# Kernel optimization log

Measured on AMD Instinct MI355X. Metric: run time of the kernel, lower is better.

Reference implementation:

```python
import jax, jax.numpy as jnp
import numpy as np
import math

ROPE_BASE = 10000.0
ALIBI_SLOPE = 2.0 ** (-8.0)  # _get_alibi_slopes(1) == [2**(-8*1/1)]


def _rope_cos_sin(T, d):
    inv_freq = 1.0 / (ROPE_BASE ** (jnp.arange(0, d, 2, dtype=jnp.float32) / d))
    t = jnp.arange(T, dtype=jnp.float32)
    freqs = jnp.einsum('i,j->ij', t, inv_freq)          # [T, d/2]
    emb = jnp.concatenate([freqs, freqs], axis=-1)      # [T, d]
    return jnp.cos(emb), jnp.sin(emb)


def _rotate_half(x):
    x1, x2 = jnp.split(x, 2, axis=-1)
    return jnp.concatenate([-x2, x1], axis=-1)


def setup_inputs() -> dict:
    key = jax.random.key(0)
    kq, kk, kv = jax.random.split(key, 3)
    B, T, H = 8, 2048, 256
    return {
        'q': jax.random.normal(kq, (B, T, H), dtype=jnp.float32),
        'k': jax.random.normal(kk, (B, T, H), dtype=jnp.float32),
        'v': jax.random.normal(kv, (B, T, H), dtype=jnp.float32),
    }


def reference(q, k, v):
    B, T, H = q.shape  # num_heads == 1, so head_dim == H
    cos, sin = _rope_cos_sin(T, H)                      # [T, H]
    qe = q * cos + _rotate_half(q) * sin                # [B, T, H]
    ke = k * cos + _rotate_half(k) * sin                # [B, T, H]

    scale = 1.0 / math.sqrt(H)
    scores = jnp.einsum('btd,bsd->bts', qe, ke) * scale  # [B, T, T]

    pos = jnp.arange(T)
    rel = (pos[None, :] - pos[:, None]).astype(jnp.float32)  # [T, T]
    alibi = (ALIBI_SLOPE * rel)[None, None, :, :]            # [1, 1, T, T]

    # torch broadcast: [B,T,T] + [1,1,T,T] -> [1,B,T,T]
    scores = scores + alibi
    attn = jax.nn.softmax(scores, axis=-1)              # [1, B, T, T]
    out = jnp.matmul(attn, v)                           # [1, B, T, H]
    return out
```

## Files before the change

kernel.cpp:

```cpp
#include <hip/hip_runtime.h>

#define B_ 8
#define T_ 2048
#define H_ 256
#define PSTR 40
#define SCALE2 0.0901684403f
#define SLOPE2 0.00563552752f
#define ELEMS ((size_t)B_ * T_ * H_)

typedef __attribute__((ext_vector_type(8))) short bf16x8;
typedef __attribute__((ext_vector_type(4))) float f32x4;

#define MFMA16(a, b, c) __builtin_amdgcn_mfma_f32_16x16x32_bf16((a), (b), (c), 0, 0, 0)

__device__ __forceinline__ ushort f2bf(float f) {
  unsigned u = __float_as_uint(f);
  u += 0x7FFFu + ((u >> 16) & 1u);
  return (ushort)(u >> 16);
}

__device__ __forceinline__ void gl_lds16(const ushort* g, ushort* l) {
  __builtin_amdgcn_global_load_lds(
      (const __attribute__((address_space(1))) unsigned int*)g,
      (__attribute__((address_space(3))) unsigned int*)l, 16, 0, 0);
}

__global__ void prep_kernel(const float* __restrict__ k, const float* __restrict__ v,
                            ushort* __restrict__ kt, ushort* __restrict__ vt) {
  __shared__ ushort tile[64][72];
  const int bid = blockIdx.x;
  const int tid = threadIdx.x;
  if (bid < 1024) {
    int idx = bid * 256 + tid;
    int d8 = idx & 15;
    int bt = idx >> 4;
    int t = bt & (T_ - 1);
    int b = bt >> 11;
    size_t base = (size_t)bt * H_ + d8 * 8;
    float4 a0 = *(const float4*)(k + base);
    float4 a1 = *(const float4*)(k + base + 4);
    float4 c0 = *(const float4*)(k + base + 128);
    float4 c1 = *(const float4*)(k + base + 132);
    float av[8] = {a0.x, a0.y, a0.z, a0.w, a1.x, a1.y, a1.z, a1.w};
    float cv[8] = {c0.x, c0.y, c0.z, c0.w, c1.x, c1.y, c1.z, c1.w};
    bf16x8 lo, hi;
#pragma unroll
    for (int e = 0; e < 8; ++e) {
      int j = d8 * 8 + e;
      float rv = (float)t * exp2f((float)j * -0.103810252959f) * 0.15915494309f;
      float fr = rv - floorf(rv);
      float sn = __builtin_amdgcn_sinf(fr), cs = __builtin_amdgcn_cosf(fr);
      lo[e] = (short)f2bf(av[e] * cs - cv[e] * sn);
      hi[e] = (short)f2bf(cv[e] * cs + av[e] * sn);
    }
    size_t kdst = (((size_t)(b * 64 + (t >> 5)) * 32 + d8) * 32 + (t & 31)) * 8;
    *(bf16x8*)(kt + kdst) = lo;
    *(bf16x8*)(kt + kdst + 4096) = hi;
  } else {
    int bid2 = bid - 1024;
    int b = bid2 >> 7, rem = bid2 & 127;
    int h0 = (rem >> 5) * 64, t0 = (rem & 31) * 64;
    int c4 = tid & 15, r0 = tid >> 4;
#pragma unroll
    for (int p = 0; p < 4; ++p) {
      int row = r0 + p * 16;
      const float4 f = *(const float4*)(v + ((size_t)(b * T_ + t0 + row)) * H_ + h0 + c4 * 4);
      ushort4 u;
      u.x = f2bf(f.x); u.y = f2bf(f.y); u.z = f2bf(f.z); u.w = f2bf(f.w);
      *(ushort4*)&tile[row][(c4 * 4) ^ (8 * ((row >> 3) & 7))] = u;
    }
    __syncthreads();
#pragma unroll
    for (int p = 0; p < 2; ++p) {
      int c = tid + p * 256;
      int h = c >> 3, tc = (c & 7) * 8;
      int xo = 8 * (c & 7);
      ushort4 u0, u1;
      u0.x = tile[tc + 0][h ^ xo]; u0.y = tile[tc + 1][h ^ xo];
      u0.z = tile[tc + 2][h ^ xo]; u0.w = tile[tc + 3][h ^ xo];
      u1.x = tile[tc + 4][h ^ xo]; u1.y = tile[tc + 5][h ^ xo];
      u1.z = tile[tc + 6][h ^ xo]; u1.w = tile[tc + 7][h ^ xo];
      int tg = t0 + tc;
      size_t dst = (((size_t)(b * 64 + (tg >> 5)) * 4 + ((tg >> 3) & 3)) * 256 + (h0 + h)) * 8;
      *(ushort4*)(vt + dst) = u0;
      *(ushort4*)(vt + dst + 4) = u1;
    }
  }
}

__global__ __launch_bounds__(512, 4)
void attn_kernel(const float* __restrict__ q, const ushort* __restrict__ kt,
                 const ushort* __restrict__ vt, float* __restrict__ out,
                 float* __restrict__ opart, float* __restrict__ lpart) {
  __shared__ ushort Ksh[2][8192];
  __shared__ ushort Vsh[2][8192];
  __shared__ ushort Psh[8][16 * PSTR];

  const int tid = threadIdx.x;
  const int w = tid >> 6, lane = tid & 63, quad = lane >> 4, l16 = lane & 15;
  const int b = blockIdx.x;
  const int q0 = blockIdx.y * 128;
  const int sp = blockIdx.z;
  const int S = gridDim.z;
  const int niter = (T_ / 32) / S;
  const int kvb = sp * (T_ / S);

  bf16x8 aq[8];
  {
    const float* qb = q + ((size_t)(b * T_) + q0 + w * 16) * H_;
    const int t = q0 + w * 16 + l16;
    float qv[8][8];
#pragma unroll
    for (int ks = 0; ks < 8; ++ks) {
      float4 x0 = *(const float4*)(qb + (size_t)l16 * H_ + ks * 32 + quad * 8);
      float4 x1 = *(const float4*)(qb + (size_t)l16 * H_ + ks * 32 + quad * 8 + 4);
      qv[ks][0] = x0.x; qv[ks][1] = x0.y; qv[ks][2] = x0.z; qv[ks][3] = x0.w;
      qv[ks][4] = x1.x; qv[ks][5] = x1.y; qv[ks][6] = x1.z; qv[ks][7] = x1.w;
    }
#pragma unroll
    for (int ks = 0; ks < 4; ++ks)
#pragma unroll
      for (int e = 0; e < 8; ++e) {
        int d = ks * 32 + quad * 8 + e;
        float rv = (float)t * exp2f((float)d * -0.103810252959f) * 0.15915494309f;
        float fr = rv - floorf(rv);
        float sn = __builtin_amdgcn_sinf(fr), cs = __builtin_amdgcn_cosf(fr);
        aq[ks][e]     = (short)f2bf(qv[ks][e] * cs - qv[ks + 4][e] * sn);
        aq[ks + 4][e] = (short)f2bf(qv[ks + 4][e] * cs + qv[ks][e] * sn);
      }
  }

  const f32x4 fzero = {0.f, 0.f, 0.f, 0.f};
  f32x4 O[16], lac = fzero;
#pragma unroll
  for (int ht = 0; ht < 16; ++ht) O[ht] = fzero;
  bf16x8 vones;
#pragma unroll
  for (int i = 0; i < 8; ++i) vones[i] = (short)0x3F80;

  const ushort* ktb = kt + (size_t)(b * 64 + sp * niter) * 8192;
  const ushort* vtb = vt + (size_t)(b * 64 + sp * niter) * 8192;
  const int stoff = tid * 8;

#pragma unroll
  for (int tt = 0; tt < 2; ++tt) {
    const ushort* kg = ktb + (size_t)tt * 8192;
    const ushort* vg = vtb + (size_t)tt * 8192;
    gl_lds16(kg + stoff, &Ksh[tt][stoff]);
    gl_lds16(kg + stoff + 4096, &Ksh[tt][stoff + 4096]);
    gl_lds16(vg + stoff, &Vsh[tt][stoff]);
    gl_lds16(vg + stoff + 4096, &Vsh[tt][stoff + 4096]);
  }

  const float arb = SLOPE2 * (float)(q0 + w * 16 + quad * 4);

  for (int it = 0; it < niter; ++it) {
    const int p = it & 1;
    __builtin_amdgcn_sched_barrier(0);
    if (it == niter - 1) __builtin_amdgcn_s_waitcnt(0x0070);
    else                 __builtin_amdgcn_s_waitcnt(0x0F74);
    __builtin_amdgcn_s_barrier();
    __builtin_amdgcn_sched_barrier(0);

    f32x4 s[2] = {fzero, fzero};
#pragma unroll
    for (int ks = 0; ks < 8; ++ks)
#pragma unroll
      for (int nt = 0; nt < 2; ++nt) {
        bf16x8 kf = *(const bf16x8*)&Ksh[p][((ks * 4 + quad) * 32 + nt * 16 + l16) * 8];
        s[nt] = MFMA16(aq[ks], kf, s[nt]);
      }

#pragma unroll
    for (int nt = 0; nt < 2; ++nt) {
      float ac = SLOPE2 * (float)(kvb + it * 32 + nt * 16 + l16);
#pragma unroll
      for (int r = 0; r < 4; ++r) {
        float a0 = ac - arb - SLOPE2 * (float)r;
        float pv = __builtin_amdgcn_exp2f(fmaf(s[nt][r], SCALE2, a0));
        Psh[w][(quad * 4 + r) * PSTR + nt * 16 + l16] = f2bf(pv);
      }
    }

    bf16x8 pf = *(const bf16x8*)&Psh[w][l16 * PSTR + quad * 8];
    lac = MFMA16(pf, vones, lac);
#pragma unroll
    for (int ht = 0; ht < 16; ++ht) {
      bf16x8 vf = *(const bf16x8*)&Vsh[p][(quad * 256 + ht * 16 + l16) * 8];
      O[ht] = MFMA16(pf, vf, O[ht]);
    }

    __builtin_amdgcn_sched_barrier(0);
    __builtin_amdgcn_s_waitcnt(0xC07F);
    __builtin_amdgcn_s_barrier();
    __builtin_amdgcn_sched_barrier(0);

    if (it < niter - 2) {
      const ushort* kg = ktb + (size_t)(it + 2) * 8192;
      const ushort* vg = vtb + (size_t)(it + 2) * 8192;
      gl_lds16(kg + stoff, &Ksh[p][stoff]);
      gl_lds16(kg + stoff + 4096, &Ksh[p][stoff + 4096]);
      gl_lds16(vg + stoff, &Vsh[p][stoff]);
      gl_lds16(vg + stoff + 4096, &Vsh[p][stoff + 4096]);
    }
  }

  float* od = (sp == 0) ? out : (opart + (size_t)(sp - 1) * ELEMS);
  float* ob = od + ((size_t)(b * T_) + q0 + w * 16) * H_;
#pragma unroll
  for (int r = 0; r < 4; ++r) {
    int row = quad * 4 + r;
#pragma unroll
    for (int ht = 0; ht < 16; ++ht)
      ob[(size_t)row * H_ + ht * 16 + l16] = O[ht][r];
  }
  if (l16 == 0) {
#pragma unroll
    for (int r = 0; r < 4; ++r)
      lpart[(size_t)(sp * B_ + b) * T_ + q0 + w * 16 + quad * 4 + r] = lac[r];
  }
}

__global__ void combine_kernel(float* __restrict__ out, const float* __restrict__ opart,
                               const float* __restrict__ lpart, int S) {
  int idx = blockIdx.x * 256 + threadIdx.x;
  int row = idx >> 6;
  float l = lpart[row];
  for (int s = 1; s < S; ++s) l += lpart[(size_t)s * B_ * T_ + row];
  float inv = 1.0f / l;
  float4 a = ((const float4*)out)[idx];
  for (int s = 1; s < S; ++s) {
    float4 c = ((const float4*)opart)[(size_t)(s - 1) * (ELEMS / 4) + idx];
    a.x += c.x; a.y += c.y; a.z += c.z; a.w += c.w;
  }
  a.x *= inv; a.y *= inv; a.z *= inv; a.w *= inv;
  ((float4*)out)[idx] = a;
}

extern "C" void kernel_launch(void* const* d_in, const int* in_sizes, int n_in,
                              void* d_out, int out_size, void* d_ws, size_t ws_size,
                              hipStream_t stream) {
  const float* q = (const float*)d_in[0];
  const float* k = (const float*)d_in[1];
  const float* v = (const float*)d_in[2];
  float* out = (float*)d_out;

  ushort* kt = (ushort*)d_ws;
  ushort* vt = kt + ELEMS;
  float* opart = (float*)(vt + ELEMS);
  const size_t need4 = ELEMS * 4 + 3 * ELEMS * 4 + (size_t)4 * B_ * T_ * 4;
  const int S = (ws_size >= need4) ? 4 : 2;
  float* lpart = opart + (size_t)(S - 1) * ELEMS;

  prep_kernel<<<dim3(2048), 256, 0, stream>>>(k, v, kt, vt);
  attn_kernel<<<dim3(B_, T_ / 128, S), 512, 0, stream>>>(q, kt, vt, out, opart, lpart);
  combine_kernel<<<dim3((B_ * T_ * H_ / 4) / 256), 256, 0, stream>>>(out, opart, lpart, S);
}
```

Measured before the change: 153.4 us.

## Split KV range across wave groups inside block and merge in LDS, dropping combine kernel

The attention kernel now processes 64 query rows per block, with two groups of four waves each covering half of the KV sequence. The two partial outputs and row sums are merged through shared memory, and the result is written directly. This removes the partial-output workspace traffic and the separate combine kernel launch. In exchange it uses about 138 KB of LDS per block, so only one block fits per CU, and the grid is 2048 blocks with less latency hiding across blocks.

```diff
diff --git a/kernel.cpp b/kernel.cpp
--- a/kernel.cpp
+++ b/kernel.cpp
@@ -88,27 +88,33 @@
   }
 }
 
-__global__ __launch_bounds__(512, 4)
+__global__ __launch_bounds__(512, 1)
 void attn_kernel(const float* __restrict__ q, const ushort* __restrict__ kt,
-                 const ushort* __restrict__ vt, float* __restrict__ out,
-                 float* __restrict__ opart, float* __restrict__ lpart) {
-  __shared__ ushort Ksh[2][8192];
-  __shared__ ushort Vsh[2][8192];
-  __shared__ ushort Psh[8][16 * PSTR];
+                 const ushort* __restrict__ vt, float* __restrict__ out) {
+  __shared__ __align__(16) char smem[141568];
+  ushort* Kbase = (ushort*)smem;
+  ushort* Vbase = (ushort*)(smem + 65536);
+  ushort* Pbase = (ushort*)(smem + 131072);
+  float*  Lsh   = (float*)(smem + 141312);
+  float*  Ofl   = (float*)smem;
 
   const int tid = threadIdx.x;
   const int w = tid >> 6, lane = tid & 63, quad = lane >> 4, l16 = lane & 15;
+  const int g = w >> 2;
+  const int wl = w & 3;
+  const int gt = tid & 255;
   const int b = blockIdx.x;
-  const int q0 = blockIdx.y * 128;
-  const int sp = blockIdx.z;
-  const int S = gridDim.z;
-  const int niter = (T_ / 32) / S;
-  const int kvb = sp * (T_ / S);
+  const int q0 = blockIdx.y * 64;
+  const int kvb0 = g * (T_ / 2);
+
+  ushort* Ksh = Kbase + g * 16384;
+  ushort* Vsh = Vbase + g * 16384;
+  ushort* Psh = Pbase + w * (16 * PSTR);
 
   bf16x8 aq[8];
   {
-    const float* qb = q + ((size_t)(b * T_) + q0 + w * 16) * H_;
-    const int t = q0 + w * 16 + l16;
+    const float* qb = q + ((size_t)(b * T_) + q0 + wl * 16) * H_;
+    const int t = q0 + wl * 16 + l16;
     float qv[8][8];
 #pragma unroll
     for (int ks = 0; ks < 8; ++ks) {
@@ -138,27 +144,28 @@
 #pragma unroll
   for (int i = 0; i < 8; ++i) vones[i] = (short)0x3F80;
 
-  const ushort* ktb = kt + (size_t)(b * 64 + sp * niter) * 8192;
-  const ushort* vtb = vt + (size_t)(b * 64 + sp * niter) * 8192;
-  const int stoff = tid * 8;
+  const ushort* ktb = kt + (size_t)(b * 64 + g * 32) * 8192;
+  const ushort* vtb = vt + (size_t)(b * 64 + g * 32) * 8192;
+  const int stoff = gt * 8;
 
 #pragma unroll
   for (int tt = 0; tt < 2; ++tt) {
     const ushort* kg = ktb + (size_t)tt * 8192;
     const ushort* vg = vtb + (size_t)tt * 8192;
-    gl_lds16(kg + stoff, &Ksh[tt][stoff]);
-    gl_lds16(kg + stoff + 4096, &Ksh[tt][stoff + 4096]);
-    gl_lds16(vg + stoff, &Vsh[tt][stoff]);
-    gl_lds16(vg + stoff + 4096, &Vsh[tt][stoff + 4096]);
-  }
-
-  const float arb = SLOPE2 * (float)(q0 + w * 16 + quad * 4);
-
-  for (int it = 0; it < niter; ++it) {
+#pragma unroll
+    for (int i = 0; i < 4; ++i) {
+      gl_lds16(kg + stoff + i * 2048, Ksh + tt * 8192 + stoff + i * 2048);
+      gl_lds16(vg + stoff + i * 2048, Vsh + tt * 8192 + stoff + i * 2048);
+    }
+  }
+
+  const float arb = SLOPE2 * (float)(q0 + wl * 16 + quad * 4);
+
+  for (int it = 0; it < 32; ++it) {
     const int p = it & 1;
     __builtin_amdgcn_sched_barrier(0);
-    if (it == niter - 1) __builtin_amdgcn_s_waitcnt(0x0070);
-    else                 __builtin_amdgcn_s_waitcnt(0x0F74);
+    if (it == 31) __builtin_amdgcn_s_waitcnt(0x0070);
+    else          __builtin_amdgcn_s_waitcnt(0x0F78);
     __builtin_amdgcn_s_barrier();
     __builtin_amdgcn_sched_barrier(0);
 
@@ -167,26 +174,26 @@
     for (int ks = 0; ks < 8; ++ks)
 #pragma unroll
       for (int nt = 0; nt < 2; ++nt) {
-        bf16x8 kf = *(const bf16x8*)&Ksh[p][((ks * 4 + quad) * 32 + nt * 16 + l16) * 8];
+        bf16x8 kf = *(const bf16x8*)&Ksh[p * 8192 + ((ks * 4 + quad) * 32 + nt * 16 + l16) * 8];
         s[nt] = MFMA16(aq[ks], kf, s[nt]);
       }
 
 #pragma unroll
     for (int nt = 0; nt < 2; ++nt) {
-      float ac = SLOPE2 * (float)(kvb + it * 32 + nt * 16 + l16);
+      float ac = SLOPE2 * (float)(kvb0 + it * 32 + nt * 16 + l16);
 #pragma unroll
       for (int r = 0; r < 4; ++r) {
         float a0 = ac - arb - SLOPE2 * (float)r;
         float pv = __builtin_amdgcn_exp2f(fmaf(s[nt][r], SCALE2, a0));
-        Psh[w][(quad * 4 + r) * PSTR + nt * 16 + l16] = f2bf(pv);
-      }
-    }
-
-    bf16x8 pf = *(const bf16x8*)&Psh[w][l16 * PSTR + quad * 8];
+        Psh[(quad * 4 + r) * PSTR + nt * 16 + l16] = f2bf(pv);
+      }
+    }
+
+    bf16x8 pf = *(const bf16x8*)&Psh[l16 * PSTR + quad * 8];
     lac = MFMA16(pf, vones, lac);
 #pragma unroll
     for (int ht = 0; ht < 16; ++ht) {
-      bf16x8 vf = *(const bf16x8*)&Vsh[p][(quad * 256 + ht * 16 + l16) * 8];
+      bf16x8 vf = *(const bf16x8*)&Vsh[p * 8192 + (quad * 256 + ht * 16 + l16) * 8];
       O[ht] = MFMA16(pf, vf, O[ht]);
     }
 
@@ -195,46 +202,40 @@
     __builtin_amdgcn_s_barrier();
     __builtin_amdgcn_sched_barrier(0);
 
-    if (it < niter - 2) {
+    if (it < 30) {
       const ushort* kg = ktb + (size_t)(it + 2) * 8192;
       const ushort* vg = vtb + (size_t)(it + 2) * 8192;
-      gl_lds16(kg + stoff, &Ksh[p][stoff]);
-      gl_lds16(kg + stoff + 4096, &Ksh[p][stoff + 4096]);
-      gl_lds16(vg + stoff, &Vsh[p][stoff]);
-      gl_lds16(vg + stoff + 4096, &Vsh[p][stoff + 4096]);
-    }
-  }
-
-  float* od = (sp == 0) ? out : (opart + (size_t)(sp - 1) * ELEMS);
-  float* ob = od + ((size_t)(b * T_) + q0 + w * 16) * H_;
-#pragma unroll
-  for (int r = 0; r < 4; ++r) {
-    int row = quad * 4 + r;
-#pragma unroll
-    for (int ht = 0; ht < 16; ++ht)
-      ob[(size_t)row * H_ + ht * 16 + l16] = O[ht][r];
-  }
-  if (l16 == 0) {
-#pragma unroll
-    for (int r = 0; r < 4; ++r)
-      lpart[(size_t)(sp * B_ + b) * T_ + q0 + w * 16 + quad * 4 + r] = lac[r];
-  }
-}
-
-__global__ void combine_kernel(float* __restrict__ out, const float* __restrict__ opart,
-                               const float* __restrict__ lpart, int S) {
-  int idx = blockIdx.x * 256 + threadIdx.x;
-  int row = idx >> 6;
-  float l = lpart[row];
-  for (int s = 1; s < S; ++s) l += lpart[(size_t)s * B_ * T_ + row];
-  float inv = 1.0f / l;
-  float4 a = ((const float4*)out)[idx];
-  for (int s = 1; s < S; ++s) {
-    float4 c = ((const float4*)opart)[(size_t)(s - 1) * (ELEMS / 4) + idx];
-    a.x += c.x; a.y += c.y; a.z += c.z; a.w += c.w;
-  }
-  a.x *= inv; a.y *= inv; a.z *= inv; a.w *= inv;
-  ((float4*)out)[idx] = a;
+#pragma unroll
+      for (int i = 0; i < 4; ++i) {
+        gl_lds16(kg + stoff + i * 2048, Ksh + p * 8192 + stoff + i * 2048);
+        gl_lds16(vg + stoff + i * 2048, Vsh + p * 8192 + stoff + i * 2048);
+      }
+    }
+  }
+
+  if (g == 1) {
+#pragma unroll
+    for (int r = 0; r < 4; ++r) {
+      int row = wl * 16 + quad * 4 + r;
+#pragma unroll
+      for (int ht = 0; ht < 16; ++ht)
+        Ofl[row * 260 + ht * 16 + l16] = O[ht][r];
+      if (l16 == 0) Lsh[row] = lac[r];
+    }
+  }
+  __syncthreads();
+  if (g == 0) {
+    float* ob = out + ((size_t)(b * T_) + q0 + wl * 16) * H_;
+#pragma unroll
+    for (int r = 0; r < 4; ++r) {
+      int row = wl * 16 + quad * 4 + r;
+      float inv = 1.0f / (lac[r] + Lsh[row]);
+#pragma unroll
+      for (int ht = 0; ht < 16; ++ht)
+        ob[(size_t)(quad * 4 + r) * H_ + ht * 16 + l16] =
+            (O[ht][r] + Ofl[row * 260 + ht * 16 + l16]) * inv;
+    }
+  }
 }
 
 extern "C" void kernel_launch(void* const* d_in, const int* in_sizes, int n_in,
@@ -247,12 +248,7 @@
 
   ushort* kt = (ushort*)d_ws;
   ushort* vt = kt + ELEMS;
-  float* opart = (float*)(vt + ELEMS);
-  const size_t need4 = ELEMS * 4 + 3 * ELEMS * 4 + (size_t)4 * B_ * T_ * 4;
-  const int S = (ws_size >= need4) ? 4 : 2;
-  float* lpart = opart + (size_t)(S - 1) * ELEMS;
 
   prep_kernel<<<dim3(2048), 256, 0, stream>>>(k, v, kt, vt);
-  attn_kernel<<<dim3(B_, T_ / 128, S), 512, 0, stream>>>(q, kt, vt, out, opart, lpart);
-  combine_kernel<<<dim3((B_ * T_ * H_ / 4) / 256), 256, 0, stream>>>(out, opart, lpart, S);
-}
+  attn_kernel<<<dim3(B_, T_ / 64), 512, 0, stream>>>(q, kt, vt, out);
+}
```

New measurement: 144.6 us. 5.7% less time.

## Double KV tile to 64 keys and fix split-K at two partitions

Applied to the files above, without the earlier changes.

Each attention iteration now processes 64 keys instead of 32, doubling the K/V LDS buffers (about 64KB each for double buffering) and the P scratch stride. The split-K factor is hardwired to 2, which halves the partial-output traffic and simplifies the combine kernel. The intent is fewer barriers and waits per key and less combine memory traffic. The cost is higher LDS usage, which cuts occupancy (launch bounds drop to 2 blocks per SM), and fewer blocks in the grid.

```diff
diff --git a/kernel.cpp b/kernel.cpp
--- a/kernel.cpp
+++ b/kernel.cpp
@@ -3,7 +3,7 @@
 #define B_ 8
 #define T_ 2048
 #define H_ 256
-#define PSTR 40
+#define PSTR 72
 #define SCALE2 0.0901684403f
 #define SLOPE2 0.00563552752f
 #define ELEMS ((size_t)B_ * T_ * H_)
@@ -88,12 +88,12 @@
   }
 }
 
-__global__ __launch_bounds__(512, 4)
+__global__ __launch_bounds__(512, 2)
 void attn_kernel(const float* __restrict__ q, const ushort* __restrict__ kt,
                  const ushort* __restrict__ vt, float* __restrict__ out,
-                 float* __restrict__ opart, float* __restrict__ lpart) {
-  __shared__ ushort Ksh[2][8192];
-  __shared__ ushort Vsh[2][8192];
+                 float* __restrict__ o1, float* __restrict__ lpart) {
+  __shared__ ushort Ksh[2][16384];
+  __shared__ ushort Vsh[2][16384];
   __shared__ ushort Psh[8][16 * PSTR];
 
   const int tid = threadIdx.x;
@@ -101,9 +101,8 @@
   const int b = blockIdx.x;
   const int q0 = blockIdx.y * 128;
   const int sp = blockIdx.z;
-  const int S = gridDim.z;
-  const int niter = (T_ / 32) / S;
-  const int kvb = sp * (T_ / S);
+  const int kvb = sp * (T_ / 2);
+  const int niter = 16;
 
   bf16x8 aq[8];
   {
@@ -138,18 +137,19 @@
 #pragma unroll
   for (int i = 0; i < 8; ++i) vones[i] = (short)0x3F80;
 
-  const ushort* ktb = kt + (size_t)(b * 64 + sp * niter) * 8192;
-  const ushort* vtb = vt + (size_t)(b * 64 + sp * niter) * 8192;
+  const ushort* ktb = kt + (size_t)(b * 64 + sp * 32) * 8192;
+  const ushort* vtb = vt + (size_t)(b * 64 + sp * 32) * 8192;
   const int stoff = tid * 8;
 
 #pragma unroll
   for (int tt = 0; tt < 2; ++tt) {
-    const ushort* kg = ktb + (size_t)tt * 8192;
-    const ushort* vg = vtb + (size_t)tt * 8192;
-    gl_lds16(kg + stoff, &Ksh[tt][stoff]);
-    gl_lds16(kg + stoff + 4096, &Ksh[tt][stoff + 4096]);
-    gl_lds16(vg + stoff, &Vsh[tt][stoff]);
-    gl_lds16(vg + stoff + 4096, &Vsh[tt][stoff + 4096]);
+    const ushort* kg = ktb + (size_t)tt * 16384;
+    const ushort* vg = vtb + (size_t)tt * 16384;
+#pragma unroll
+    for (int i = 0; i < 4; ++i) {
+      gl_lds16(kg + stoff + i * 4096, &Ksh[tt][stoff + i * 4096]);
+      gl_lds16(vg + stoff + i * 4096, &Vsh[tt][stoff + i * 4096]);
+    }
   }
 
   const float arb = SLOPE2 * (float)(q0 + w * 16 + quad * 4);
@@ -158,22 +158,23 @@
     const int p = it & 1;
     __builtin_amdgcn_sched_barrier(0);
     if (it == niter - 1) __builtin_amdgcn_s_waitcnt(0x0070);
-    else                 __builtin_amdgcn_s_waitcnt(0x0F74);
+    else                 __builtin_amdgcn_s_waitcnt(0x0F78);
     __builtin_amdgcn_s_barrier();
     __builtin_amdgcn_sched_barrier(0);
 
-    f32x4 s[2] = {fzero, fzero};
+    f32x4 s[4] = {fzero, fzero, fzero, fzero};
 #pragma unroll
     for (int ks = 0; ks < 8; ++ks)
 #pragma unroll
-      for (int nt = 0; nt < 2; ++nt) {
-        bf16x8 kf = *(const bf16x8*)&Ksh[p][((ks * 4 + quad) * 32 + nt * 16 + l16) * 8];
+      for (int nt = 0; nt < 4; ++nt) {
+        bf16x8 kf = *(const bf16x8*)&Ksh[p][(nt >> 1) * 8192 +
+            ((ks * 4 + quad) * 32 + (nt & 1) * 16 + l16) * 8];
         s[nt] = MFMA16(aq[ks], kf, s[nt]);
       }
 
 #pragma unroll
-    for (int nt = 0; nt < 2; ++nt) {
-      float ac = SLOPE2 * (float)(kvb + it * 32 + nt * 16 + l16);
+    for (int nt = 0; nt < 4; ++nt) {
+      float ac = SLOPE2 * (float)(kvb + it * 64 + nt * 16 + l16);
 #pragma unroll
       for (int r = 0; r < 4; ++r) {
         float a0 = ac - arb - SLOPE2 * (float)r;
@@ -182,12 +183,16 @@
       }
     }
 
-    bf16x8 pf = *(const bf16x8*)&Psh[w][l16 * PSTR + quad * 8];
-    lac = MFMA16(pf, vones, lac);
+    bf16x8 pf0 = *(const bf16x8*)&Psh[w][l16 * PSTR + quad * 8];
+    bf16x8 pf1 = *(const bf16x8*)&Psh[w][l16 * PSTR + 32 + quad * 8];
+    lac = MFMA16(pf0, vones, lac);
+    lac = MFMA16(pf1, vones, lac);
 #pragma unroll
     for (int ht = 0; ht < 16; ++ht) {
-      bf16x8 vf = *(const bf16x8*)&Vsh[p][(quad * 256 + ht * 16 + l16) * 8];
-      O[ht] = MFMA16(pf, vf, O[ht]);
+      bf16x8 vf0 = *(const bf16x8*)&Vsh[p][(quad * 256 + ht * 16 + l16) * 8];
+      bf16x8 vf1 = *(const bf16x8*)&Vsh[p][8192 + (quad * 256 + ht * 16 + l16) * 8];
+      O[ht] = MFMA16(pf0, vf0, O[ht]);
+      O[ht] = MFMA16(pf1, vf1, O[ht]);
     }
 
     __builtin_amdgcn_sched_barrier(0);
@@ -196,16 +201,17 @@
     __builtin_amdgcn_sched_barrier(0);
 
     if (it < niter - 2) {
-      const ushort* kg = ktb + (size_t)(it + 2) * 8192;
-      const ushort* vg = vtb + (size_t)(it + 2) * 8192;
-      gl_lds16(kg + stoff, &Ksh[p][stoff]);
-      gl_lds16(kg + stoff + 4096, &Ksh[p][stoff + 4096]);
-      gl_lds16(vg + stoff, &Vsh[p][stoff]);
-      gl_lds16(vg + stoff + 4096, &Vsh[p][stoff + 4096]);
-    }
-  }
-
-  float* od = (sp == 0) ? out : (opart + (size_t)(sp - 1) * ELEMS);
+      const ushort* kg = ktb + (size_t)(it + 2) * 16384;
+      const ushort* vg = vtb + (size_t)(it + 2) * 16384;
+#pragma unroll
+      for (int i = 0; i < 4; ++i) {
+        gl_lds16(kg + stoff + i * 4096, &Ksh[p][stoff + i * 4096]);
+        gl_lds16(vg + stoff + i * 4096, &Vsh[p][stoff + i * 4096]);
+      }
+    }
+  }
+
+  float* od = (sp == 0) ? out : o1;
   float* ob = od + ((size_t)(b * T_) + q0 + w * 16) * H_;
 #pragma unroll
   for (int r = 0; r < 4; ++r) {
@@ -221,19 +227,15 @@
   }
 }
 
-__global__ void combine_kernel(float* __restrict__ out, const float* __restrict__ opart,
-                               const float* __restrict__ lpart, int S) {
+__global__ void combine_kernel(float* __restrict__ out, const float* __restrict__ o1,
+                               const float* __restrict__ lpart) {
   int idx = blockIdx.x * 256 + threadIdx.x;
   int row = idx >> 6;
-  float l = lpart[row];
-  for (int s = 1; s < S; ++s) l += lpart[(size_t)s * B_ * T_ + row];
-  float inv = 1.0f / l;
+  float inv = 1.0f / (lpart[row] + lpart[B_ * T_ + row]);
   float4 a = ((const float4*)out)[idx];
-  for (int s = 1; s < S; ++s) {
-    float4 c = ((const float4*)opart)[(size_t)(s - 1) * (ELEMS / 4) + idx];
-    a.x += c.x; a.y += c.y; a.z += c.z; a.w += c.w;
-  }
-  a.x *= inv; a.y *= inv; a.z *= inv; a.w *= inv;
+  float4 c = ((const float4*)o1)[idx];
+  a.x = (a.x + c.x) * inv; a.y = (a.y + c.y) * inv;
+  a.z = (a.z + c.z) * inv; a.w = (a.w + c.w) * inv;
   ((float4*)out)[idx] = a;
 }
 
@@ -247,12 +249,10 @@
 
   ushort* kt = (ushort*)d_ws;
   ushort* vt = kt + ELEMS;
-  float* opart = (float*)(vt + ELEMS);
-  const size_t need4 = ELEMS * 4 + 3 * ELEMS * 4 + (size_t)4 * B_ * T_ * 4;
-  const int S = (ws_size >= need4) ? 4 : 2;
-  float* lpart = opart + (size_t)(S - 1) * ELEMS;
+  float* o1 = (float*)(vt + ELEMS);
+  float* lpart = o1 + ELEMS;
 
   prep_kernel<<<dim3(2048), 256, 0, stream>>>(k, v, kt, vt);
-  attn_kernel<<<dim3(B_, T_ / 128, S), 512, 0, stream>>>(q, kt, vt, out, opart, lpart);
-  combine_kernel<<<dim3((B_ * T_ * H_ / 4) / 256), 256, 0, stream>>>(out, opart, lpart, S);
-}
+  attn_kernel<<<dim3(B_, T_ / 128, 2), 512, 0, stream>>>(q, kt, vt, out, o1, lpart);
+  combine_kernel<<<dim3((B_ * T_ * H_ / 4) / 256), 256, 0, stream>>>(out, o1, lpart);
+}
```

Result: faster. 145.5 us (-5.2%).

## Switch attention to 32x32x16 MFMA with 32-row query tiles per wave

Applied to the files above, without the earlier changes.

Each wave now handles 32 query rows with the 32x32x16 bf16 MFMA instead of 16 rows with 16x16x32. Each block covers 256 queries, halving the grid along T and halving how often each K/V tile is streamed into LDS per query. This raises MFMA work per LDS load. In exchange the accumulator registers roughly double, so launch bounds drop to 2 blocks per SM, which lowers occupancy and the latency hiding it gives.

```diff
diff --git a/kernel.cpp b/kernel.cpp
--- a/kernel.cpp
+++ b/kernel.cpp
@@ -10,8 +10,9 @@
 
 typedef __attribute__((ext_vector_type(8))) short bf16x8;
 typedef __attribute__((ext_vector_type(4))) float f32x4;
-
-#define MFMA16(a, b, c) __builtin_amdgcn_mfma_f32_16x16x32_bf16((a), (b), (c), 0, 0, 0)
+typedef __attribute__((ext_vector_type(16))) float f32x16;
+
+#define MFMA32(a, b, c) __builtin_amdgcn_mfma_f32_32x32x16_bf16((a), (b), (c), 0, 0, 0)
 
 __device__ __forceinline__ ushort f2bf(float f) {
   unsigned u = __float_as_uint(f);
@@ -88,58 +89,62 @@
   }
 }
 
-__global__ __launch_bounds__(512, 4)
+__global__ __launch_bounds__(512, 2)
 void attn_kernel(const float* __restrict__ q, const ushort* __restrict__ kt,
                  const ushort* __restrict__ vt, float* __restrict__ out,
                  float* __restrict__ opart, float* __restrict__ lpart) {
   __shared__ ushort Ksh[2][8192];
   __shared__ ushort Vsh[2][8192];
-  __shared__ ushort Psh[8][16 * PSTR];
+  __shared__ ushort Psh[8][32 * PSTR];
 
   const int tid = threadIdx.x;
-  const int w = tid >> 6, lane = tid & 63, quad = lane >> 4, l16 = lane & 15;
+  const int w = tid >> 6, lane = tid & 63;
+  const int l31 = lane & 31, lh = lane >> 5;
   const int b = blockIdx.x;
-  const int q0 = blockIdx.y * 128;
+  const int q0 = blockIdx.y * 256;
   const int sp = blockIdx.z;
   const int S = gridDim.z;
   const int niter = (T_ / 32) / S;
   const int kvb = sp * (T_ / S);
 
-  bf16x8 aq[8];
+  bf16x8 aq[16];
   {
-    const float* qb = q + ((size_t)(b * T_) + q0 + w * 16) * H_;
-    const int t = q0 + w * 16 + l16;
-    float qv[8][8];
+    const float* qb = q + ((size_t)(b * T_) + q0 + w * 32 + l31) * H_;
+    const float tq = (float)(q0 + w * 32 + l31);
 #pragma unroll
     for (int ks = 0; ks < 8; ++ks) {
-      float4 x0 = *(const float4*)(qb + (size_t)l16 * H_ + ks * 32 + quad * 8);
-      float4 x1 = *(const float4*)(qb + (size_t)l16 * H_ + ks * 32 + quad * 8 + 4);
-      qv[ks][0] = x0.x; qv[ks][1] = x0.y; qv[ks][2] = x0.z; qv[ks][3] = x0.w;
-      qv[ks][4] = x1.x; qv[ks][5] = x1.y; qv[ks][6] = x1.z; qv[ks][7] = x1.w;
-    }
-#pragma unroll
-    for (int ks = 0; ks < 4; ++ks)
+      const float* pl = qb + ks * 16 + lh * 8;
+      float4 x0 = *(const float4*)(pl);
+      float4 x1 = *(const float4*)(pl + 4);
+      float4 y0 = *(const float4*)(pl + 128);
+      float4 y1 = *(const float4*)(pl + 132);
+      float lo[8] = {x0.x, x0.y, x0.z, x0.w, x1.x, x1.y, x1.z, x1.w};
+      float hi[8] = {y0.x, y0.y, y0.z, y0.w, y1.x, y1.y, y1.z, y1.w};
 #pragma unroll
       for (int e = 0; e < 8; ++e) {
-        int d = ks * 32 + quad * 8 + e;
-        float rv = (float)t * exp2f((float)d * -0.103810252959f) * 0.15915494309f;
+        int d = ks * 16 + lh * 8 + e;
+        float rv = tq * exp2f((float)d * -0.103810252959f) * 0.15915494309f;
         float fr = rv - floorf(rv);
         float sn = __builtin_amdgcn_sinf(fr), cs = __builtin_amdgcn_cosf(fr);
-        aq[ks][e]     = (short)f2bf(qv[ks][e] * cs - qv[ks + 4][e] * sn);
-        aq[ks + 4][e] = (short)f2bf(qv[ks + 4][e] * cs + qv[ks][e] * sn);
+        aq[ks][e]     = (short)f2bf(lo[e] * cs - hi[e] * sn);
+        aq[ks + 8][e] = (short)f2bf(hi[e] * cs + lo[e] * sn);
       }
-  }
-
-  const f32x4 fzero = {0.f, 0.f, 0.f, 0.f};
-  f32x4 O[16], lac = fzero;
-#pragma unroll
-  for (int ht = 0; ht < 16; ++ht) O[ht] = fzero;
+    }
+  }
+
+  f32x16 fz16;
+#pragma unroll
+  for (int i = 0; i < 16; ++i) fz16[i] = 0.f;
+  f32x16 O[8], lac;
+#pragma unroll
+  for (int hb = 0; hb < 8; ++hb) O[hb] = fz16;
+  lac = fz16;
   bf16x8 vones;
 #pragma unroll
   for (int i = 0; i < 8; ++i) vones[i] = (short)0x3F80;
 
-  const ushort* ktb = kt + (size_t)(b * 64 + sp * niter) * 8192;
-  const ushort* vtb = vt + (size_t)(b * 64 + sp * niter) * 8192;
+  const ushort* ktb = kt + (size_t)(b * 64 + sp * (64 / S)) * 8192;
+  const ushort* vtb = vt + (size_t)(b * 64 + sp * (64 / S)) * 8192;
   const int stoff = tid * 8;
 
 #pragma unroll
@@ -152,7 +157,7 @@
     gl_lds16(vg + stoff + 4096, &Vsh[tt][stoff + 4096]);
   }
 
-  const float arb = SLOPE2 * (float)(q0 + w * 16 + quad * 4);
+  const float arb2 = SLOPE2 * (float)(q0 + w * 32);
 
   for (int it = 0; it < niter; ++it) {
     const int p = it & 1;
@@ -162,32 +167,33 @@
     __builtin_amdgcn_s_barrier();
     __builtin_amdgcn_sched_barrier(0);
 
-    f32x4 s[2] = {fzero, fzero};
-#pragma unroll
-    for (int ks = 0; ks < 8; ++ks)
-#pragma unroll
-      for (int nt = 0; nt < 2; ++nt) {
-        bf16x8 kf = *(const bf16x8*)&Ksh[p][((ks * 4 + quad) * 32 + nt * 16 + l16) * 8];
-        s[nt] = MFMA16(aq[ks], kf, s[nt]);
+    f32x16 s = fz16;
+#pragma unroll
+    for (int ks = 0; ks < 16; ++ks) {
+      bf16x8 kf = *(const bf16x8*)&Ksh[p][(((ks * 2 + lh) * 32) + l31) * 8];
+      s = MFMA32(aq[ks], kf, s);
+    }
+
+    {
+      float ac = SLOPE2 * (float)(kvb + it * 32 + l31) - arb2;
+#pragma unroll
+      for (int r = 0; r < 16; ++r) {
+        int row = (r & 3) + 8 * (r >> 2) + 4 * lh;
+        float pv = __builtin_amdgcn_exp2f(fmaf(s[r], SCALE2, ac - SLOPE2 * (float)row));
+        Psh[w][row * PSTR + l31] = f2bf(pv);
       }
-
-#pragma unroll
-    for (int nt = 0; nt < 2; ++nt) {
-      float ac = SLOPE2 * (float)(kvb + it * 32 + nt * 16 + l16);
-#pragma unroll
-      for (int r = 0; r < 4; ++r) {
-        float a0 = ac - arb - SLOPE2 * (float)r;
-        float pv = __builtin_amdgcn_exp2f(fmaf(s[nt][r], SCALE2, a0));
-        Psh[w][(quad * 4 + r) * PSTR + nt * 16 + l16] = f2bf(pv);
-      }
-    }
-
-    bf16x8 pf = *(const bf16x8*)&Psh[w][l16 * PSTR + quad * 8];
-    lac = MFMA16(pf, vones, lac);
-#pragma unroll
-    for (int ht = 0; ht < 16; ++ht) {
-      bf16x8 vf = *(const bf16x8*)&Vsh[p][(quad * 256 + ht * 16 + l16) * 8];
-      O[ht] = MFMA16(pf, vf, O[ht]);
+    }
+
+    bf16x8 pf0 = *(const bf16x8*)&Psh[w][l31 * PSTR + lh * 8];
+    bf16x8 pf1 = *(const bf16x8*)&Psh[w][l31 * PSTR + 16 + lh * 8];
+    lac = MFMA32(pf0, vones, lac);
+    lac = MFMA32(pf1, vones, lac);
+#pragma unroll
+    for (int hb = 0; hb < 8; ++hb) {
+      bf16x8 vf0 = *(const bf16x8*)&Vsh[p][((lh * 256) + hb * 32 + l31) * 8];
+      bf16x8 vf1 = *(const bf16x8*)&Vsh[p][(((2 + lh) * 256) + hb * 32 + l31) * 8];
+      O[hb] = MFMA32(pf0, vf0, O[hb]);
+      O[hb] = MFMA32(pf1, vf1, O[hb]);
     }
 
     __builtin_amdgcn_sched_barrier(0);
@@ -206,18 +212,20 @@
   }
 
   float* od = (sp == 0) ? out : (opart + (size_t)(sp - 1) * ELEMS);
-  float* ob = od + ((size_t)(b * T_) + q0 + w * 16) * H_;
-#pragma unroll
-  for (int r = 0; r < 4; ++r) {
-    int row = quad * 4 + r;
-#pragma unroll
-    for (int ht = 0; ht < 16; ++ht)
-      ob[(size_t)row * H_ + ht * 16 + l16] = O[ht][r];
-  }
-  if (l16 == 0) {
-#pragma unroll
-    for (int r = 0; r < 4; ++r)
-      lpart[(size_t)(sp * B_ + b) * T_ + q0 + w * 16 + quad * 4 + r] = lac[r];
+  float* ob = od + ((size_t)(b * T_) + q0 + w * 32) * H_;
+#pragma unroll
+  for (int r = 0; r < 16; ++r) {
+    int row = (r & 3) + 8 * (r >> 2) + 4 * lh;
+#pragma unroll
+    for (int hb = 0; hb < 8; ++hb)
+      ob[(size_t)row * H_ + hb * 32 + l31] = O[hb][r];
+  }
+  if (l31 == 0) {
+#pragma unroll
+    for (int r = 0; r < 16; ++r) {
+      int row = (r & 3) + 8 * (r >> 2) + 4 * lh;
+      lpart[(size_t)(sp * B_ + b) * T_ + q0 + w * 32 + row] = lac[r];
+    }
   }
 }
 
@@ -253,6 +261,6 @@
   float* lpart = opart + (size_t)(S - 1) * ELEMS;
 
   prep_kernel<<<dim3(2048), 256, 0, stream>>>(k, v, kt, vt);
-  attn_kernel<<<dim3(B_, T_ / 128, S), 512, 0, stream>>>(q, kt, vt, out, opart, lpart);
+  attn_kernel<<<dim3(B_, T_ / 256, S), 512, 0, stream>>>(q, kt, vt, out, opart, lpart);
   combine_kernel<<<dim3((B_ * T_ * H_ / 4) / 256), 256, 0, stream>>>(out, opart, lpart, S);
 }
```

After: 160.0 us. 1.04x slower.
